# Optimization experiments

Hardware: AMD Instinct MI355X
Metric: run time of the kernel (lower is better)

## Reference

```python
import jax, jax.numpy as jnp
import numpy as np

B, TX, TY = 32, 64, 64
E = H = 1024
VEN = VCN = 32000


def _lstm_scan(x_gates, Whh, bhh, h0, c0):
    # x_gates: [T, B, 4H] precomputed input contribution (x @ Wih.T + bih)
    def step(carry, xg_t):
        h, c = carry
        gates = xg_t + h @ Whh.T + bhh  # [B, 4H]
        i, f, g, o = jnp.split(gates, 4, axis=-1)  # torch gate order i,f,g,o
        c = jax.nn.sigmoid(f) * c + jax.nn.sigmoid(i) * jnp.tanh(g)
        h = jax.nn.sigmoid(o) * jnp.tanh(c)
        return (h, c), (h, c)
    (hT, cT), (hs, cs) = jax.lax.scan(step, (h0, c0), x_gates)
    return hs, cs, hT, cT  # hs/cs: [T, B, H]


def setup_inputs() -> dict:
    key = jax.random.key(0)
    ks = jax.random.split(key, 12)
    u = lambda k, shp, s: jax.random.uniform(k, shp, jnp.float32, -s, s)
    s = 1.0 / np.sqrt(H)
    return {
        "x": jax.random.randint(ks[0], (B, TX), 0, VEN, dtype=jnp.int32),
        "x_mask": jnp.ones((B, TX), dtype=jnp.int32),
        "y": jax.random.randint(ks[1], (B, TY), 0, VCN, dtype=jnp.int32),
        "h0": jnp.zeros((B, H), jnp.float32),
        "c0": jnp.zeros((B, H), jnp.float32),
        "emb_en": u(ks[2], (VEN, E), 0.1),
        "emb_cn": u(ks[3], (VCN, E), 0.1),
        "Wih_e": u(ks[4], (4 * H, E), s),
        "Whh_e": u(ks[5], (4 * H, H), s),
        "bih_e": jnp.zeros((4 * H,), jnp.float32),
        "bhh_e": jnp.zeros((4 * H,), jnp.float32),
        "Wih_d": u(ks[6], (4 * H, E), s),
        "Whh_d": u(ks[7], (4 * H, H), s),
        "bih_d": jnp.zeros((4 * H,), jnp.float32),
        "bhh_d": jnp.zeros((4 * H,), jnp.float32),
        "Wout": u(ks[8], (VCN, H), 0.1),
        "bout": jnp.zeros((VCN,), jnp.float32),
    }


def reference(x, x_mask, y, h0, c0, emb_en, emb_cn,
              Wih_e, Whh_e, bih_e, bhh_e,
              Wih_d, Whh_d, bih_d, bhh_d, Wout, bout):
    # --- encoder: per-timestep LSTMCell unrolled via lax.scan ---
    xe = emb_en[x]  # [B, Tx, E]
    xg = jnp.einsum('bte,ge->tbg', xe, Wih_e) + bih_e  # [Tx, B, 4H]
    hs, cs, _, _ = _lstm_scan(xg, Whh_e, bhh_e, h0, c0)  # [Tx, B, H]
    # pick hidden/cell at last valid timestep (mask.sum - 1)
    lengths = jnp.sum(x_mask, axis=1) - 1  # [B]
    bidx = jnp.arange(x.shape[0])
    h = hs[lengths, bidx]  # [B, H]
    c = cs[lengths, bidx]
    # --- decoder: single-layer LSTM ---
    ye = emb_cn[y]  # [B, Ty, E]
    yg = jnp.einsum('bte,ge->tbg', ye, Wih_d) + bih_d  # [Ty, B, 4H]
    dh, _, _, _ = _lstm_scan(yg, Whh_d, bhh_d, h, c)  # [Ty, B, H]
    hiddens = jnp.transpose(dh, (1, 0, 2))  # [B, Ty, H]
    logits = jnp.einsum('bth,vh->btv', hiddens, Wout) + bout  # [B, Ty, V]
    decoded = jax.nn.log_softmax(logits, axis=-1)
    return decoded, hiddens
```

## Files before the change

kernel.cpp:

```cpp
#include <hip/hip_runtime.h>

typedef __attribute__((ext_vector_type(8))) short bf16x8;
typedef __attribute__((ext_vector_type(4))) float fx4;
typedef __attribute__((ext_vector_type(4))) unsigned short u16x4;
typedef __attribute__((ext_vector_type(8))) unsigned short u16x8;
typedef __attribute__((ext_vector_type(4))) unsigned int u32x4;

#define DEV static __device__ __forceinline__

DEV unsigned short f2bf(float f) {
  union { float f; unsigned u; } v; v.f = f;
  unsigned u = v.u;
  u += 0x7fffu + ((u >> 16) & 1u);
  return (unsigned short)(u >> 16);
}
DEV unsigned pk(float a, float b) { return (unsigned)f2bf(a) | ((unsigned)f2bf(b) << 16); }
DEV float sigm(float x) { return 1.f / (1.f + __expf(-x)); }

DEV u32x4 load_coh16(const void* p) {
  u32x4 r;
  asm volatile("global_load_dwordx4 %0, %1, off sc0 sc1" : "=v"(r) : "v"(p));
  return r;
}

typedef __attribute__((address_space(1))) const unsigned int guint;
typedef __attribute__((address_space(3))) unsigned int luint;
DEV void gload_lds16(const void* g, void* l) {
  __builtin_amdgcn_global_load_lds((guint*)g, (luint*)l, 16, 0, 0);
}

__global__ void k_gather2(const float* __restrict__ embE, const int* __restrict__ tokE,
                          unsigned short* __restrict__ dstE,
                          const float* __restrict__ embC, const int* __restrict__ tokC,
                          unsigned short* __restrict__ dstC) {
  int bid = blockIdx.x;
  int r = bid & 2047;
  const float* emb = bid < 2048 ? embE : embC;
  const int* tok = bid < 2048 ? tokE : tokC;
  unsigned short* dst = bid < 2048 ? dstE : dstC;
  int t = r >> 5, b = r & 31;
  int token = tok[b * 64 + t];
  const fx4* srow = (const fx4*)(emb + (long)token * 1024);
  u16x4* drow = (u16x4*)(dst + (long)r * 1024);
  fx4 v = srow[threadIdx.x];
  u16x4 o = { f2bf(v[0]), f2bf(v[1]), f2bf(v[2]), f2bf(v[3]) };
  drow[threadIdx.x] = o;
}

__global__ void k_lengths(const int* __restrict__ mask, int* __restrict__ sel,
                          int* __restrict__ bar) {
  int t = threadIdx.x;
  for (int i = t; i < 4096; i += 256) bar[i] = 0;
  if (t < 32) {
    int s = 0;
    for (int k = 0; k < 64; ++k) s += mask[t * 64 + k];
    sel[t] = (s + 63) & 63;
  }
}

__global__ void k_f2bf_dual(const float* __restrict__ s0, unsigned short* __restrict__ d0,
                            const float* __restrict__ s1, unsigned short* __restrict__ d1,
                            long n4) {
  const float* s = blockIdx.x < 1024 ? s0 : s1;
  unsigned short* d = blockIdx.x < 1024 ? d0 : d1;
  long base = (long)(blockIdx.x & 1023) * 256 + threadIdx.x;
  for (long i = base; i < n4; i += 1024 * 256) {
    fx4 v = ((const fx4*)s)[i];
    u16x4 o = { f2bf(v[0]), f2bf(v[1]), f2bf(v[2]), f2bf(v[3]) };
    ((u16x4*)d)[i] = o;
  }
}

#define SCAN_NBLK 128

template<int MODE>
__global__ __launch_bounds__(512) void k_scan(
    const float* __restrict__ Whh,
    const float* __restrict__ bhh,
    const float* __restrict__ xg,
    const float* __restrict__ hinit,
    const float* __restrict__ cinit,
    unsigned short* __restrict__ hbuf,
    const int* __restrict__ sel,
    float* __restrict__ hsel, float* __restrict__ csel,
    float* __restrict__ hid_out,
    unsigned short* __restrict__ hid_bf,
    int* __restrict__ bar,
    const float* __restrict__ wsrc,
    unsigned short* __restrict__ wdst,
    long wn4) {
  int tid = threadIdx.x;
  int bid = blockIdx.x;
  if (bid >= SCAN_NBLK) {
    long i = (long)(bid - SCAN_NBLK) * 512 + tid;
    long st = (long)(gridDim.x - SCAN_NBLK) * 512;
    for (; i < wn4; i += st) {
      fx4 v = ((const fx4*)wsrc)[i];
      u16x4 o = { f2bf(v[0]), f2bf(v[1]), f2bf(v[2]), f2bf(v[3]) };
      ((u16x4*)wdst)[i] = o;
    }
    return;
  }
  __shared__ __align__(16) unsigned short hlds[49152];
  __shared__ float gbuf[2][2][32][16];
  int j0 = ((bid & 7) * 16 + (bid >> 3)) * 8;
  int w = tid >> 6, lane = tid & 63;
  int mt = w & 1, nt = (w >> 1) & 1, kh = w >> 2;
  int fr = lane & 15, fg = lane >> 4;
  unsigned* hbU = (unsigned*)hbuf;
  constexpr int GBASE = MODE ? 64 : 0;

  bf16x8 breg[16];
  {
    int r = nt * 16 + fr;
    const float* wrow = Whh + ((long)((r >> 3) * 1024 + j0 + (r & 7)) << 10);
#pragma unroll
    for (int i = 0; i < 16; ++i) {
      int kc = (kh * 16 + i) * 4 + fg;
      fx4 lo = *(const fx4*)(wrow + kc * 8);
      fx4 hi = *(const fx4*)(wrow + kc * 8 + 4);
      bf16x8 o = { (short)f2bf(lo[0]), (short)f2bf(lo[1]), (short)f2bf(lo[2]), (short)f2bf(lo[3]),
                   (short)f2bf(hi[0]), (short)f2bf(hi[1]), (short)f2bf(hi[2]), (short)f2bf(hi[3]) };
      breg[i] = o;
    }
  }

  int b = (tid & 255) >> 3, jj = tid & 7, j = j0 + jj;
  float bh0 = 0.f, bh1 = 0.f, bh2 = 0.f, bh3 = 0.f, c_reg = 0.f;
  float x0 = 0.f, x1 = 0.f, x2 = 0.f, x3 = 0.f;
  int sel_b = -1;
  if (tid < 256) {
    bh0 = bhh[j]; bh1 = bhh[1024 + j]; bh2 = bhh[2048 + j]; bh3 = bhh[3072 + j];
    c_reg = cinit[b * 1024 + j];
    if (MODE == 0) sel_b = sel[b];
    const float* xp = xg + (long)b * 4096 + j;
    x0 = xp[0]; x1 = xp[1024]; x2 = xp[2048]; x3 = xp[3072];
  }

  for (int t = 0; t < 64; ++t) {
    if (t == 0) {
#pragma unroll
      for (int it = 0; it < 8; ++it) {
        int c = it * 512 + tid;
        const float* src = hinit + (long)c * 8;
        fx4 lo = *(const fx4*)src;
        fx4 hi = *(const fx4*)(src + 4);
        int row = c >> 7, kc = c & 127;
        u16x8 o = { f2bf(lo[0]), f2bf(lo[1]), f2bf(lo[2]), f2bf(lo[3]),
                    f2bf(hi[0]), f2bf(hi[1]), f2bf(hi[2]), f2bf(hi[3]) };
        *(u16x8*)&hlds[(row * 128 + (kc ^ (row & 31))) * 8] = o;
      }
    } else {
      const char* hsrc = (const char*)hbuf + (t & 1) * 65536;
      u32x4 hv[8];
#pragma unroll
      for (int it = 0; it < 8; ++it) {
        int c = it * 512 + tid;
        hv[it] = load_coh16(hsrc + (long)c * 16);
      }
      asm volatile("s_waitcnt vmcnt(0)" ::: "memory");
      __builtin_amdgcn_sched_barrier(0);
#pragma unroll
      for (int it = 0; it < 8; ++it) {
        int c = it * 512 + tid;
        int row = c >> 7, kc = c & 127;
        *(u16x8*)&hlds[(row * 128 + (kc ^ (row & 31))) * 8] = *(u16x8*)&hv[it];
      }
    }
    __syncthreads();

    int arow = mt * 16 + fr;
    fx4 acca = {0.f, 0.f, 0.f, 0.f}, accb = {0.f, 0.f, 0.f, 0.f};
#pragma unroll
    for (int i = 0; i < 16; i += 2) {
      int kcA = (kh * 16 + i) * 4 + fg;
      int kcB = (kh * 16 + i + 1) * 4 + fg;
      bf16x8 a0 = *(const bf16x8*)&hlds[(arow * 128 + (kcA ^ (arow & 31))) * 8];
      bf16x8 a1 = *(const bf16x8*)&hlds[(arow * 128 + (kcB ^ (arow & 31))) * 8];
      acca = __builtin_amdgcn_mfma_f32_16x16x32_bf16(a0, breg[i], acca, 0, 0, 0);
      accb = __builtin_amdgcn_mfma_f32_16x16x32_bf16(a1, breg[i + 1], accb, 0, 0, 0);
    }
#pragma unroll
    for (int q = 0; q < 4; ++q)
      gbuf[kh][nt][mt * 16 + fg * 4 + q][fr] = acca[q] + accb[q];
    __syncthreads();

    if (tid < 256) {
      float gi = gbuf[0][0][b][jj]     + gbuf[1][0][b][jj]     + bh0 + x0;
      float gf = gbuf[0][0][b][8 + jj] + gbuf[1][0][b][8 + jj] + bh1 + x1;
      float gg = gbuf[0][1][b][jj]     + gbuf[1][1][b][jj]     + bh2 + x2;
      float go = gbuf[0][1][b][8 + jj] + gbuf[1][1][b][8 + jj] + bh3 + x3;
      float c_new = sigm(gf) * c_reg + sigm(gi) * tanhf(gg);
      float h = sigm(go) * tanhf(c_new);
      c_reg = c_new;
      float hp = __shfl_xor(h, 1);
      if ((jj & 1) == 0) {
        unsigned val = pk(h, hp);
        __hip_atomic_store(&hbU[((t & 1) ^ 1) * 16384 + b * 512 + ((j0 + jj) >> 1)], val,
                           __ATOMIC_RELAXED, __HIP_MEMORY_SCOPE_AGENT);
      }
      if (MODE == 0) {
        if (t == sel_b) { hsel[b * 1024 + j] = h; csel[b * 1024 + j] = c_new; }
      } else {
        long o = ((long)b * 64 + t) * 1024 + j;
        hid_out[o] = h;
        if (hid_bf) hid_bf[o] = f2bf(h);
      }
    }

    if (t < 63) {
      float nx0 = 0.f, nx1 = 0.f, nx2 = 0.f, nx3 = 0.f;
      if (tid < 256) {
        const float* xp = xg + (long)(t + 1) * 131072 + (long)b * 4096 + j;
        nx0 = xp[0]; nx1 = xp[1024]; nx2 = xp[2048]; nx3 = xp[3072];
      }
      __syncthreads();
      if (w == 0) {
        if (lane == 0)
          __hip_atomic_store(&bar[bid * 32], GBASE + t + 1, __ATOMIC_RELAXED, __HIP_MEMORY_SCOPE_AGENT);
        int want = GBASE + t + 1;
        for (;;) {
          int v0 = __hip_atomic_load(&bar[lane * 32], __ATOMIC_RELAXED, __HIP_MEMORY_SCOPE_AGENT);
          int v1 = __hip_atomic_load(&bar[(64 + lane) * 32], __ATOMIC_RELAXED, __HIP_MEMORY_SCOPE_AGENT);
          if (__ballot(v0 >= want && v1 >= want) == 0xFFFFFFFFFFFFFFFFULL) break;
          __builtin_amdgcn_s_sleep(1);
        }
      }
      __syncthreads();
      x0 = nx0; x1 = nx1; x2 = nx2; x3 = nx3;
    }
  }
}

__global__ __launch_bounds__(256) void k_gemm_dual(
    const unsigned short* __restrict__ A0, const unsigned short* __restrict__ B0,
    const float* __restrict__ bias0, float* __restrict__ C0,
    const unsigned short* __restrict__ A1, const unsigned short* __restrict__ B1,
    const float* __restrict__ bias1, float* __restrict__ C1) {
  __shared__ __align__(16) unsigned short As[2][4096];
  __shared__ __align__(16) unsigned short Bs[2][4096];
  int lid = blockIdx.x;
  int half = lid >> 9, l = lid & 511;
  const unsigned short* A = half ? A1 : A0;
  const unsigned short* Bw = half ? B1 : B0;
  const float* bias = half ? bias1 : bias0;
  float* C = half ? C1 : C0;
  int swz = (l & 7) * 64 + (l >> 3);
  long m0 = (long)(swz & 15) * 128;
  long n0 = (long)(swz >> 4) * 128;
  int tid = threadIdx.x, lane = tid & 63, w = tid >> 6;
  int mw = (w & 1) * 64, nw = (w >> 1) * 64;
  int fr = lane & 15, fg = lane >> 4;
  fx4 acc[4][4] = {};
  int c0 = tid, c1 = tid + 256;
  int r0 = c0 >> 2, k0s = (c0 & 3) ^ ((r0 >> 1) & 3);
  int r1 = c1 >> 2, k1s = (c1 & 3) ^ ((r1 >> 1) & 3);
  const unsigned short* gA0 = A + (m0 + r0) * 1024 + k0s * 8;
  const unsigned short* gA1 = A + (m0 + r1) * 1024 + k1s * 8;
  const unsigned short* gB0 = Bw + (n0 + r0) * 1024 + k0s * 8;
  const unsigned short* gB1 = Bw + (n0 + r1) * 1024 + k1s * 8;
  auto stage = [&](int buf, int kt) {
    int k0 = kt * 32;
    gload_lds16(gA0 + k0, &As[buf][c0 * 8]);
    gload_lds16(gA1 + k0, &As[buf][c1 * 8]);
    gload_lds16(gB0 + k0, &Bs[buf][c0 * 8]);
    gload_lds16(gB1 + k0, &Bs[buf][c1 * 8]);
  };
  stage(0, 0);
  __syncthreads();
  for (int kt = 0; kt < 32; ++kt) {
    int cur = kt & 1;
    if (kt < 31) stage(cur ^ 1, kt + 1);
    bf16x8 af[4], bfr[4];
#pragma unroll
    for (int mi = 0; mi < 4; ++mi) {
      int row = mw + mi * 16 + fr;
      af[mi] = *(const bf16x8*)&As[cur][(row * 4 + (fg ^ ((row >> 1) & 3))) * 8];
    }
#pragma unroll
    for (int ni = 0; ni < 4; ++ni) {
      int row = nw + ni * 16 + fr;
      bfr[ni] = *(const bf16x8*)&Bs[cur][(row * 4 + (fg ^ ((row >> 1) & 3))) * 8];
    }
#pragma unroll
    for (int mi = 0; mi < 4; ++mi)
#pragma unroll
      for (int ni = 0; ni < 4; ++ni)
        acc[mi][ni] = __builtin_amdgcn_mfma_f32_16x16x32_bf16(af[mi], bfr[ni], acc[mi][ni], 0, 0, 0);
    __syncthreads();
  }
#pragma unroll
  for (int ni = 0; ni < 4; ++ni) {
    long n = n0 + nw + ni * 16 + fr;
    float bs = bias[n];
#pragma unroll
    for (int mi = 0; mi < 4; ++mi) {
      long rbase = m0 + mw + mi * 16 + fg * 4;
#pragma unroll
      for (int q = 0; q < 4; ++q)
        C[(rbase + q) * 4096 + n] = acc[mi][ni][q] + bs;
    }
  }
}

__global__ __launch_bounds__(256) void k_gemm_bb(const unsigned short* __restrict__ A,
                                                 const unsigned short* __restrict__ Bw,
                                                 const float* __restrict__ bias,
                                                 float* __restrict__ C) {
  __shared__ __align__(16) unsigned short As[2][4096];
  __shared__ __align__(16) unsigned short Bs[2][4096];
  int lid = blockIdx.x;
  int swz = (lid & 7) * 500 + (lid >> 3);
  long m0 = (long)(swz & 15) * 128;
  long n0 = (long)(swz >> 4) * 128;
  int tid = threadIdx.x, lane = tid & 63, w = tid >> 6;
  int mw = (w & 1) * 64, nw = (w >> 1) * 64;
  int fr = lane & 15, fg = lane >> 4;
  fx4 acc[4][4] = {};
  int c0 = tid, c1 = tid + 256;
  int r0 = c0 >> 2, k0s = (c0 & 3) ^ ((r0 >> 1) & 3);
  int r1 = c1 >> 2, k1s = (c1 & 3) ^ ((r1 >> 1) & 3);
  const unsigned short* gA0 = A + (m0 + r0) * 1024 + k0s * 8;
  const unsigned short* gA1 = A + (m0 + r1) * 1024 + k1s * 8;
  const unsigned short* gB0 = Bw + (n0 + r0) * 1024 + k0s * 8;
  const unsigned short* gB1 = Bw + (n0 + r1) * 1024 + k1s * 8;
  auto stage = [&](int buf, int kt) {
    int k0 = kt * 32;
    gload_lds16(gA0 + k0, &As[buf][c0 * 8]);
    gload_lds16(gA1 + k0, &As[buf][c1 * 8]);
    gload_lds16(gB0 + k0, &Bs[buf][c0 * 8]);
    gload_lds16(gB1 + k0, &Bs[buf][c1 * 8]);
  };
  stage(0, 0);
  __syncthreads();
  for (int kt = 0; kt < 32; ++kt) {
    int cur = kt & 1;
    if (kt < 31) stage(cur ^ 1, kt + 1);
    bf16x8 af[4], bfr[4];
#pragma unroll
    for (int mi = 0; mi < 4; ++mi) {
      int row = mw + mi * 16 + fr;
      af[mi] = *(const bf16x8*)&As[cur][(row * 4 + (fg ^ ((row >> 1) & 3))) * 8];
    }
#pragma unroll
    for (int ni = 0; ni < 4; ++ni) {
      int row = nw + ni * 16 + fr;
      bfr[ni] = *(const bf16x8*)&Bs[cur][(row * 4 + (fg ^ ((row >> 1) & 3))) * 8];
    }
#pragma unroll
    for (int mi = 0; mi < 4; ++mi)
#pragma unroll
      for (int ni = 0; ni < 4; ++ni)
        acc[mi][ni] = __builtin_amdgcn_mfma_f32_16x16x32_bf16(af[mi], bfr[ni], acc[mi][ni], 0, 0, 0);
    __syncthreads();
  }
#pragma unroll
  for (int ni = 0; ni < 4; ++ni) {
    long n = n0 + nw + ni * 16 + fr;
    float bs = bias[n];
#pragma unroll
    for (int mi = 0; mi < 4; ++mi) {
      long rbase = m0 + mw + mi * 16 + fg * 4;
#pragma unroll
      for (int q = 0; q < 4; ++q)
        C[(rbase + q) * 32000 + n] = acc[mi][ni][q] + bs;
    }
  }
}

template<typename TA, typename TB>
__global__ __launch_bounds__(256) void k_gemm(const TA* __restrict__ A,
                                              const TB* __restrict__ Bw,
                                              const float* __restrict__ bias,
                                              float* __restrict__ C,
                                              int ldc, int q8) {
  __shared__ __align__(16) unsigned short As[2][4096];
  __shared__ __align__(16) unsigned short Bs[2][4096];
  int lid = blockIdx.x;
  int swz = (lid & 7) * q8 + (lid >> 3);
  long m0 = (long)(swz & 15) * 128;
  long n0 = (long)(swz >> 4) * 128;
  int tid = threadIdx.x, lane = tid & 63, w = tid >> 6;
  int mw = (w & 1) * 64, nw = (w >> 1) * 64;
  int fr = lane & 15, fg = lane >> 4;
  fx4 acc[4][4] = {};

  int crow[2], kc[2], phys[2];
#pragma unroll
  for (int u = 0; u < 2; ++u) {
    int c = tid + u * 256;
    crow[u] = c >> 2; kc[u] = c & 3;
    phys[u] = crow[u] * 4 + (kc[u] ^ ((crow[u] >> 1) & 3));
  }
  u32x4 ra[2], rb[2];
  auto loadOne = [&](const auto* P, long row, int u) -> u32x4 {
    long off = row * 1024 + kc[u] * 8;
    if constexpr (sizeof(*P) == 2) {
      return *(const u32x4*)(P + off);
    } else {
      fx4 lo = *(const fx4*)(P + off);
      fx4 hi = *(const fx4*)(P + off + 4);
      u32x4 r = { pk(lo[0], lo[1]), pk(lo[2], lo[3]), pk(hi[0], hi[1]), pk(hi[2], hi[3]) };
      return r;
    }
  };
  auto loadRegs = [&](int kt) {
#pragma unroll
    for (int u = 0; u < 2; ++u) {
      ra[u] = loadOne(A + (long)kt * 32, m0 + crow[u], u);
      rb[u] = loadOne(Bw + (long)kt * 32, n0 + crow[u], u);
    }
  };
  auto storeRegs = [&](int buf) {
#pragma unroll
    for (int u = 0; u < 2; ++u) {
      *(u32x4*)&As[buf][phys[u] * 8] = ra[u];
      *(u32x4*)&Bs[buf][phys[u] * 8] = rb[u];
    }
  };
  loadRegs(0);
  storeRegs(0);
  __syncthreads();
  for (int kt = 0; kt < 32; ++kt) {
    int cur = kt & 1;
    if (kt < 31) loadRegs(kt + 1);
    bf16x8 af[4], bf_[4];
#pragma unroll
    for (int mi = 0; mi < 4; ++mi) {
      int row = mw + mi * 16 + fr;
      af[mi] = *(const bf16x8*)&As[cur][(row * 4 + (fg ^ ((row >> 1) & 3))) * 8];
    }
#pragma unroll
    for (int ni = 0; ni < 4; ++ni) {
      int row = nw + ni * 16 + fr;
      bf_[ni] = *(const bf16x8*)&Bs[cur][(row * 4 + (fg ^ ((row >> 1) & 3))) * 8];
    }
#pragma unroll
    for (int mi = 0; mi < 4; ++mi)
#pragma unroll
      for (int ni = 0; ni < 4; ++ni)
        acc[mi][ni] = __builtin_amdgcn_mfma_f32_16x16x32_bf16(af[mi], bf_[ni], acc[mi][ni], 0, 0, 0);
    if (kt < 31) storeRegs((kt + 1) & 1);
    __syncthreads();
  }
#pragma unroll
  for (int ni = 0; ni < 4; ++ni) {
    long n = n0 + nw + ni * 16 + fr;
    float bs = bias[n];
#pragma unroll
    for (int mi = 0; mi < 4; ++mi) {
      long rbase = m0 + mw + mi * 16 + fg * 4;
#pragma unroll
      for (int q = 0; q < 4; ++q)
        C[(rbase + q) * ldc + n] = acc[mi][ni][q] + bs;
    }
  }
}

__global__ __launch_bounds__(256) void k_logsoftmax(float* __restrict__ logits) {
  long base = (long)blockIdx.x * 32000;
  float* row = logits + base;
  int tid = threadIdx.x;
  __shared__ float redm[4], reds[4];
  float m = -3.4e38f, s = 0.f;
  for (int i = tid; i < 8000; i += 256) {
    fx4 v = ((const fx4*)row)[i];
    float cm = fmaxf(fmaxf(v[0], v[1]), fmaxf(v[2], v[3]));
    if (cm > m) { s *= __expf(m - cm); m = cm; }
    s += __expf(v[0] - m) + __expf(v[1] - m) + __expf(v[2] - m) + __expf(v[3] - m);
  }
  for (int o = 32; o; o >>= 1) {
    float m2 = __shfl_xor(m, o), s2 = __shfl_xor(s, o);
    float mn = fmaxf(m, m2);
    s = s * __expf(m - mn) + s2 * __expf(m2 - mn);
    m = mn;
  }
  if ((tid & 63) == 0) { redm[tid >> 6] = m; reds[tid >> 6] = s; }
  __syncthreads();
  float M = fmaxf(fmaxf(redm[0], redm[1]), fmaxf(redm[2], redm[3]));
  float S = reds[0] * __expf(redm[0] - M) + reds[1] * __expf(redm[1] - M) +
            reds[2] * __expf(redm[2] - M) + reds[3] * __expf(redm[3] - M);
  float lse = M + logf(S);
  for (int i = tid; i < 8000; i += 256) {
    fx4 v = ((const fx4*)row)[i];
    fx4 o = { v[0] - lse, v[1] - lse, v[2] - lse, v[3] - lse };
    ((fx4*)row)[i] = o;
  }
}

extern "C" void kernel_launch(void* const* d_in, const int* in_sizes, int n_in,
                              void* d_out, int out_size, void* d_ws, size_t ws_size,
                              hipStream_t stream) {
  const int*   x     = (const int*)d_in[0];
  const int*   xmask = (const int*)d_in[1];
  const int*   y     = (const int*)d_in[2];
  const float* h0    = (const float*)d_in[3];
  const float* c0    = (const float*)d_in[4];
  const float* embE  = (const float*)d_in[5];
  const float* embC  = (const float*)d_in[6];
  const float* WihE  = (const float*)d_in[7];
  const float* WhhE  = (const float*)d_in[8];
  const float* bihE  = (const float*)d_in[9];
  const float* bhhE  = (const float*)d_in[10];
  const float* WihD  = (const float*)d_in[11];
  const float* WhhD  = (const float*)d_in[12];
  const float* bihD  = (const float*)d_in[13];
  const float* bhhD  = (const float*)d_in[14];
  const float* Wout  = (const float*)d_in[15];
  const float* bout  = (const float*)d_in[16];

  float* out = (float*)d_out;
  float* decoded = out;
  float* hiddens = out + 65536000L;

  float* xg_e = decoded;
  float* xg_d = decoded + 8388608L;
  unsigned short* xe_bf   = (unsigned short*)(decoded + 16777216L);
  unsigned short* ye_bf   = xe_bf + 2097152L;
  unsigned short* WihE_bf = ye_bf + 2097152L;
  unsigned short* WihD_bf = WihE_bf + 4194304L;
  char* sp = (char*)(WihD_bf + 4194304L);
  unsigned short* hbuf = (unsigned short*)sp; sp += 2 * 32768 * 2;
  float* hsel = (float*)sp; sp += 32768 * 4;
  float* csel = (float*)sp; sp += 32768 * 4;
  int* sel = (int*)sp; sp += 256;
  int* bar = (int*)sp; sp += 16384;

  unsigned short* hid_bf  = (unsigned short*)d_ws;
  unsigned short* Wout_bf = hid_bf + 2097152L;
  size_t need1 = 2048L * 1024 * 2;
  size_t need2 = need1 + 32000L * 1024 * 2;
  bool fast1 = ws_size >= need1;
  bool fast2 = ws_size >= need2;

  k_gather2<<<4096, 256, 0, stream>>>(embE, x, xe_bf, embC, y, ye_bf);
  k_lengths<<<1, 256, 0, stream>>>(xmask, sel, bar);
  k_f2bf_dual<<<2048, 256, 0, stream>>>(WihE, WihE_bf, WihD, WihD_bf, 1048576L);

  k_gemm_dual<<<1024, 256, 0, stream>>>(xe_bf, WihE_bf, bihE, xg_e,
                                        ye_bf, WihD_bf, bihD, xg_d);

  k_scan<0><<<SCAN_NBLK + (fast2 ? 112 : 0), 512, 0, stream>>>(
      WhhE, bhhE, xg_e, h0, c0, hbuf, sel, hsel, csel, nullptr, nullptr, bar,
      Wout, Wout_bf, fast2 ? 8192000L : 0L);
  k_scan<1><<<SCAN_NBLK, 512, 0, stream>>>(
      WhhD, bhhD, xg_d, hsel, csel, hbuf, nullptr, nullptr, nullptr, hiddens,
      fast1 ? hid_bf : nullptr, bar, nullptr, nullptr, 0L);

  if (fast2)      k_gemm_bb<<<4000, 256, 0, stream>>>(hid_bf, Wout_bf, bout, decoded);
  else if (fast1) k_gemm<unsigned short, float><<<4000, 256, 0, stream>>>(hid_bf, Wout, bout, decoded, 32000, 500);
  else            k_gemm<float, float><<<4000, 256, 0, stream>>>(hiddens, Wout, bout, decoded, 32000, 500);
  k_logsoftmax<<<2048, 256, 0, stream>>>(decoded);
}
```

Before: 910.2 us.

## Halve persistent LSTM scan blocks to 64 with full-K per wave

```diff
diff --git a/kernel.cpp b/kernel.cpp
--- a/kernel.cpp
+++ b/kernel.cpp
@@ -71,7 +71,7 @@
   }
 }
 
-#define SCAN_NBLK 128
+#define SCAN_NBLK 64
 
 template<int MODE>
 __global__ __launch_bounds__(512) void k_scan(
@@ -102,21 +102,20 @@
     return;
   }
   __shared__ __align__(16) unsigned short hlds[49152];
-  __shared__ float gbuf[2][2][32][16];
-  int j0 = ((bid & 7) * 16 + (bid >> 3)) * 8;
+  __shared__ float gbuf[4][32][16];
+  int j0 = ((bid & 7) * 8 + (bid >> 3)) * 16;
   int w = tid >> 6, lane = tid & 63;
-  int mt = w & 1, nt = (w >> 1) & 1, kh = w >> 2;
+  int mt = w & 1, nt = w >> 1;
   int fr = lane & 15, fg = lane >> 4;
   unsigned* hbU = (unsigned*)hbuf;
   constexpr int GBASE = MODE ? 64 : 0;
 
-  bf16x8 breg[16];
+  bf16x8 breg[32];
   {
-    int r = nt * 16 + fr;
-    const float* wrow = Whh + ((long)((r >> 3) * 1024 + j0 + (r & 7)) << 10);
-#pragma unroll
-    for (int i = 0; i < 16; ++i) {
-      int kc = (kh * 16 + i) * 4 + fg;
+    const float* wrow = Whh + ((long)(nt * 1024 + j0 + fr) << 10);
+#pragma unroll
+    for (int i = 0; i < 32; ++i) {
+      int kc = i * 4 + fg;
       fx4 lo = *(const fx4*)(wrow + kc * 8);
       fx4 hi = *(const fx4*)(wrow + kc * 8 + 4);
       bf16x8 o = { (short)f2bf(lo[0]), (short)f2bf(lo[1]), (short)f2bf(lo[2]), (short)f2bf(lo[3]),
@@ -125,17 +124,12 @@
     }
   }
 
-  int b = (tid & 255) >> 3, jj = tid & 7, j = j0 + jj;
-  float bh0 = 0.f, bh1 = 0.f, bh2 = 0.f, bh3 = 0.f, c_reg = 0.f;
-  float x0 = 0.f, x1 = 0.f, x2 = 0.f, x3 = 0.f;
-  int sel_b = -1;
-  if (tid < 256) {
-    bh0 = bhh[j]; bh1 = bhh[1024 + j]; bh2 = bhh[2048 + j]; bh3 = bhh[3072 + j];
-    c_reg = cinit[b * 1024 + j];
-    if (MODE == 0) sel_b = sel[b];
-    const float* xp = xg + (long)b * 4096 + j;
-    x0 = xp[0]; x1 = xp[1024]; x2 = xp[2048]; x3 = xp[3072];
-  }
+  int b = tid >> 4, jj = tid & 15, j = j0 + jj;
+  float bh0 = bhh[j], bh1 = bhh[1024 + j], bh2 = bhh[2048 + j], bh3 = bhh[3072 + j];
+  float c_reg = cinit[b * 1024 + j];
+  int sel_b = (MODE == 0) ? sel[b] : -1;
+  const float* xp0 = xg + (long)b * 4096 + j;
+  float x0 = xp0[0], x1 = xp0[1024], x2 = xp0[2048], x3 = xp0[3072];
 
   for (int t = 0; t < 64; ++t) {
     if (t == 0) {
@@ -172,9 +166,9 @@
     int arow = mt * 16 + fr;
     fx4 acca = {0.f, 0.f, 0.f, 0.f}, accb = {0.f, 0.f, 0.f, 0.f};
 #pragma unroll
-    for (int i = 0; i < 16; i += 2) {
-      int kcA = (kh * 16 + i) * 4 + fg;
-      int kcB = (kh * 16 + i + 1) * 4 + fg;
+    for (int i = 0; i < 32; i += 2) {
+      int kcA = i * 4 + fg;
+      int kcB = (i + 1) * 4 + fg;
       bf16x8 a0 = *(const bf16x8*)&hlds[(arow * 128 + (kcA ^ (arow & 31))) * 8];
       bf16x8 a1 = *(const bf16x8*)&hlds[(arow * 128 + (kcB ^ (arow & 31))) * 8];
       acca = __builtin_amdgcn_mfma_f32_16x16x32_bf16(a0, breg[i], acca, 0, 0, 0);
@@ -182,14 +176,14 @@
     }
 #pragma unroll
     for (int q = 0; q < 4; ++q)
-      gbuf[kh][nt][mt * 16 + fg * 4 + q][fr] = acca[q] + accb[q];
+      gbuf[nt][mt * 16 + fg * 4 + q][fr] = acca[q] + accb[q];
     __syncthreads();
 
-    if (tid < 256) {
-      float gi = gbuf[0][0][b][jj]     + gbuf[1][0][b][jj]     + bh0 + x0;
-      float gf = gbuf[0][0][b][8 + jj] + gbuf[1][0][b][8 + jj] + bh1 + x1;
-      float gg = gbuf[0][1][b][jj]     + gbuf[1][1][b][jj]     + bh2 + x2;
-      float go = gbuf[0][1][b][8 + jj] + gbuf[1][1][b][8 + jj] + bh3 + x3;
+    {
+      float gi = gbuf[0][b][jj] + bh0 + x0;
+      float gf = gbuf[1][b][jj] + bh1 + x1;
+      float gg = gbuf[2][b][jj] + bh2 + x2;
+      float go = gbuf[3][b][jj] + bh3 + x3;
       float c_new = sigm(gf) * c_reg + sigm(gi) * tanhf(gg);
       float h = sigm(go) * tanhf(c_new);
       c_reg = c_new;
@@ -209,11 +203,8 @@
     }
 
     if (t < 63) {
-      float nx0 = 0.f, nx1 = 0.f, nx2 = 0.f, nx3 = 0.f;
-      if (tid < 256) {
-        const float* xp = xg + (long)(t + 1) * 131072 + (long)b * 4096 + j;
-        nx0 = xp[0]; nx1 = xp[1024]; nx2 = xp[2048]; nx3 = xp[3072];
-      }
+      const float* xp = xg + (long)(t + 1) * 131072 + (long)b * 4096 + j;
+      float nx0 = xp[0], nx1 = xp[1024], nx2 = xp[2048], nx3 = xp[3072];
       __syncthreads();
       if (w == 0) {
         if (lane == 0)
@@ -221,8 +212,7 @@
         int want = GBASE + t + 1;
         for (;;) {
           int v0 = __hip_atomic_load(&bar[lane * 32], __ATOMIC_RELAXED, __HIP_MEMORY_SCOPE_AGENT);
-          int v1 = __hip_atomic_load(&bar[(64 + lane) * 32], __ATOMIC_RELAXED, __HIP_MEMORY_SCOPE_AGENT);
-          if (__ballot(v0 >= want && v1 >= want) == 0xFFFFFFFFFFFFFFFFULL) break;
+          if (__ballot(v0 >= want) == 0xFFFFFFFFFFFFFFFFULL) break;
           __builtin_amdgcn_s_sleep(1);
         }
       }
@@ -540,7 +530,7 @@
   k_gemm_dual<<<1024, 256, 0, stream>>>(xe_bf, WihE_bf, bihE, xg_e,
                                         ye_bf, WihD_bf, bihD, xg_d);
 
-  k_scan<0><<<SCAN_NBLK + (fast2 ? 112 : 0), 512, 0, stream>>>(
+  k_scan<0><<<SCAN_NBLK + (fast2 ? 192 : 0), 512, 0, stream>>>(
       WhhE, bhhE, xg_e, h0, c0, hbuf, sel, hsel, csel, nullptr, nullptr, bar,
       Wout, Wout_bf, fast2 ? 8192000L : 0L);
   k_scan<1><<<SCAN_NBLK, 512, 0, stream>>>(
```

Result: faster. 889.1 us (median of 2 runs) (-2.3%).
